# Kernel optimization log

Hardware: AMD Instinct MI355X
Metric: run time of the kernel (lower is better)

Reference implementation:

```python
import jax, jax.numpy as jnp
import numpy as np

B, S, D, H, AD, E = 4, 2048, 1024, 2048, 128, 8

def _ln(x, g, b, eps=1e-5):
    m = jnp.mean(x, axis=-1, keepdims=True)
    v = jnp.var(x, axis=-1, keepdims=True)
    return (x - m) * jax.lax.rsqrt(v + eps) * g + b

def setup_inputs() -> dict:
    key = jax.random.key(0)
    ks = jax.random.split(key, 12)
    scale = 1.0 / D ** 0.5
    ascale = scale * 0.01
    ead = 0.01 / AD ** 0.5
    return {
        'x': jax.random.normal(ks[0], (B, S, D), jnp.float32),
        'expert_weights': jax.random.uniform(ks[1], (B, S, E), jnp.float32),
        'Wu': jax.random.normal(ks[2], (H, D), jnp.float32) * scale,
        'bu': jnp.zeros((H,), jnp.float32),
        'Wg': jax.random.normal(ks[3], (H, D), jnp.float32) * scale,
        'bg': jnp.zeros((H,), jnp.float32),
        'Wd': jax.random.normal(ks[4], (D, H), jnp.float32) * scale,
        'bd': jnp.zeros((D,), jnp.float32),
        'Wpre': jax.random.normal(ks[5], (AD, D), jnp.float32) * ascale,
        'bpre': jnp.zeros((AD,), jnp.float32),
        'Wpost': jax.random.normal(ks[6], (AD, H), jnp.float32) * ascale,
        'bpost': jnp.zeros((AD,), jnp.float32),
        'ln_g': jnp.ones((AD,), jnp.float32),
        'ln_b': jnp.zeros((AD,), jnp.float32),
        'Wap': jax.random.normal(ks[7], (H, AD), jnp.float32) * ascale,
        'A': jax.random.normal(ks[8], (E, AD, AD), jnp.float32) * ead,
        'eg': jnp.ones((E, AD), jnp.float32),
        'eb': jnp.zeros((E, AD), jnp.float32),
        'Wp': jax.random.normal(ks[9], (H, AD), jnp.float32) * ead,
        'Wo': jax.random.normal(ks[10], (D, H), jnp.float32) * ead,
    }

def reference(x, expert_weights, Wu, bu, Wg, bg, Wd, bd, Wpre, bpre, Wpost, bpost, ln_g, ln_b, Wap, A, eg, eb, Wp, Wo):
    # ---- SharedExpertMLP ----
    up = x @ Wu.T + bu                      # [B,S,H]
    gate = x @ Wg.T + bg
    hidden = jax.nn.silu(gate) * up
    adapt_in = _ln(x @ Wpre.T + bpre, ln_g, ln_b)        # [B,S,AD]
    adapt_out = _ln(hidden @ Wpost.T + bpost, ln_g, ln_b)
    aw = jnp.einsum('bsa,bta->bst', adapt_in, adapt_out)  # [B,S,S]
    aw = jax.nn.silu(jnp.clip(aw, -5.0, 5.0))
    adapt = jnp.einsum('bst,bta->bsa', aw, adapt_in)
    hidden = hidden + 0.1 * (adapt @ Wap.T)
    shared = hidden @ Wd.T + bd                           # [B,S,D]
    # ---- expert branch (vectorized over experts) ----
    pre = x @ Wpre.T + bpre                               # [B,S,AD] (no adapt_norm here, as in torch)
    h = jnp.einsum('bsa,eca->ebsc', pre, A)               # per-expert adapter linear
    h = _ln(h, eg[:, None, None, :], eb[:, None, None, :])
    wmask = jnp.where(expert_weights > 0, expert_weights, 0.0)  # [B,S,E]
    hw = jnp.einsum('ebsa,bse->bsa', h, wmask)            # weighted combine before shared projections
    Wc = Wo @ Wp                                          # [D,AD]: output_proj(expert_proj(.))
    contrib = hw @ Wc.T                                   # [B,S,D]
    # sum_i w_i * (shared + 0.1*mask_i*expert_i) = shared*sum(w) + 0.1*sum(w_i*expert_i)
    return shared * jnp.sum(expert_weights, axis=-1, keepdims=True) + 0.1 * contrib
```

## Files before the change

kernel.cpp:

```cpp
#include <hip/hip_runtime.h>
#include <math.h>

#define BB 4
#define SS 2048
#define DD 1024
#define HH 2048
#define AD 128
#define EE 8
#define MM (BB*SS)
#define PS 136

typedef unsigned short u16;
typedef short bf16x8 __attribute__((ext_vector_type(8)));
typedef float f32x4 __attribute__((ext_vector_type(4)));
typedef float f32x16 __attribute__((ext_vector_type(16)));

__device__ __forceinline__ float silu_f(float x){ return x / (1.f + __expf(-x)); }

__device__ __forceinline__ u16 f2bf(float f){
    union { float f; unsigned u; } c; c.f = f;
    unsigned r = (c.u + 0x7FFFu + ((c.u >> 16) & 1u)) >> 16;
    return (u16)r;
}

__device__ __forceinline__ void gld16(const u16* g, u16* l){
    __builtin_amdgcn_global_load_lds((const __attribute__((address_space(1))) void*)g,
                                     (__attribute__((address_space(3))) void*)l, 16, 0, 0);
}

#define VMCNT(n) asm volatile("s_waitcnt vmcnt(" #n ")" ::: "memory")

__global__ __launch_bounds__(256,2) void mfma_sk(
    const u16* __restrict__ A, const u16* __restrict__ B, float* __restrict__ P,
    int M, int K, int S, long sA, long sB, long sC, long sSplit)
{
    __shared__ __align__(16) u16 As[128*32];
    __shared__ __align__(16) u16 Bs[128*32];
    const int t = threadIdx.x;
    const int lane = t & 63;
    const int wv = t >> 6;
    const int s = blockIdx.x;
    const int m0 = blockIdx.y * 128;
    const u16* Ab = A + (long)blockIdx.z * sA;
    const u16* Bb = B + (long)blockIdx.z * sB;
    const int srow = t >> 2, scol = (t & 3) * 8;
    const int Ks = K / S, kBeg = s * Ks;
    const u16* ga0 = Ab + (long)(m0 + srow) * K + scol + kBeg;
    const u16* ga1 = ga0 + 64L * K;
    const u16* gb0 = Bb + (long)srow * K + scol + kBeg;
    const u16* gb1 = gb0 + 64L * K;
    u16* la0 = As + t * 8;  u16* la1 = As + 2048 + t * 8;
    u16* lb0 = Bs + t * 8;  u16* lb1 = Bs + 2048 + t * 8;
    const int fr = lane & 15, q = lane >> 4;
    const int wm = (wv & 1) * 64, wn = (wv >> 1) * 64;

    f32x4 acc[4][4] = {};
    for (int k0 = 0; k0 < Ks; k0 += 32) {
        gld16(ga0 + k0, la0);
        gld16(ga1 + k0, la1);
        gld16(gb0 + k0, lb0);
        gld16(gb1 + k0, lb1);
        __syncthreads();
        bf16x8 af[4], bfr[4];
        #pragma unroll
        for (int i = 0; i < 4; ++i) af[i]  = *(const bf16x8*)&As[(wm + i*16 + fr)*32 + q*8];
        #pragma unroll
        for (int i = 0; i < 4; ++i) bfr[i] = *(const bf16x8*)&Bs[(wn + i*16 + fr)*32 + q*8];
        #pragma unroll
        for (int mi = 0; mi < 4; ++mi)
            #pragma unroll
            for (int ni = 0; ni < 4; ++ni)
                acc[mi][ni] = __builtin_amdgcn_mfma_f32_16x16x32_bf16(af[mi], bfr[ni], acc[mi][ni], 0, 0, 0);
        __syncthreads();
    }

    float* Pf = P + (long)s * sSplit + (long)blockIdx.z * sC;
    #pragma unroll
    for (int mi = 0; mi < 4; ++mi)
        #pragma unroll
        for (int ni = 0; ni < 4; ++ni) {
            const int col = wn + ni*16 + fr;
            #pragma unroll
            for (int r = 0; r < 4; ++r) {
                const int row = m0 + wm + mi*16 + q*4 + r;
                Pf[(long)row * 128 + col] = acc[mi][ni][r];
            }
        }
}

__global__ __launch_bounds__(512,2) void mfma_upgate(
    const u16* __restrict__ X, const u16* __restrict__ Wu_, const u16* __restrict__ Wg_,
    const float* __restrict__ bu, const float* __restrict__ bg, u16* __restrict__ H)
{
    __shared__ __align__(16) u16 lds[65536];
    const int t = threadIdx.x, lane = t & 63, wv = t >> 6;
    const int l31 = lane & 31, kh = lane >> 5;
    const int wr = wv >> 2, wc = wv & 3;
    const int m0 = blockIdx.y * 256, n0 = blockIdx.x * 128;

    const int srow = t >> 2;
    const int gcol = (((t & 3) ^ ((t >> 3) & 3)) * 8);
    const u16* gx0 = X   + (long)(m0 + srow) * DD + gcol;
    const u16* gx1 = gx0 + 128L * DD;
    const u16* gu  = Wu_ + (long)(n0 + srow) * DD + gcol;
    const u16* gg  = Wg_ + (long)(n0 + srow) * DD + gcol;
    const int st8 = t * 8;

    const int sw3 = (l31 >> 1) & 3;
    int offA[4][2], offB[2];
    #pragma unroll
    for (int m = 0; m < 4; ++m)
        #pragma unroll
        for (int ks = 0; ks < 2; ++ks)
            offA[m][ks] = (wr*128 + m*32 + l31)*32 + (((ks*2 + kh) ^ sw3) * 8);
    #pragma unroll
    for (int ks = 0; ks < 2; ++ks)
        offB[ks] = (wc*32 + l31)*32 + (((ks*2 + kh) ^ sw3) * 8);

    f32x16 accU[4] = {};
    f32x16 accG[4] = {};

    auto stage = [&](int tb) {
        u16* Lb = lds + (tb & 3) * 16384;
        const int k0 = tb * 32;
        gld16(gx0 + k0, Lb + st8);
        gld16(gx1 + k0, Lb + 4096 + st8);
        gld16(gu  + k0, Lb + 8192 + st8);
        gld16(gg  + k0, Lb + 12288 + st8);
    };

    auto compute = [&](int tb) {
        const u16* Lb = lds + (tb & 3) * 16384;
        bf16x8 a[4][2], uf[2], gf[2];
        #pragma unroll
        for (int ks = 0; ks < 2; ++ks) {
            uf[ks] = *(const bf16x8*)&Lb[8192  + offB[ks]];
            gf[ks] = *(const bf16x8*)&Lb[12288 + offB[ks]];
        }
        #pragma unroll
        for (int m = 0; m < 4; ++m)
            #pragma unroll
            for (int ks = 0; ks < 2; ++ks)
                a[m][ks] = *(const bf16x8*)&Lb[offA[m][ks]];
        __builtin_amdgcn_s_setprio(1);
        #pragma unroll
        for (int m = 0; m < 4; ++m)
            #pragma unroll
            for (int ks = 0; ks < 2; ++ks) {
                accU[m] = __builtin_amdgcn_mfma_f32_32x32x16_bf16(a[m][ks], uf[ks], accU[m], 0, 0, 0);
                accG[m] = __builtin_amdgcn_mfma_f32_32x32x16_bf16(a[m][ks], gf[ks], accG[m], 0, 0, 0);
            }
        __builtin_amdgcn_s_setprio(0);
    };

    stage(0); stage(1); stage(2);

    #pragma unroll 1
    for (int tt = 0; tt < 29; ++tt) {
        VMCNT(8);
        __builtin_amdgcn_s_barrier();
        __builtin_amdgcn_sched_barrier(0);
        stage(tt + 3);
        compute(tt);
    }
    VMCNT(8);
    __builtin_amdgcn_s_barrier();
    __builtin_amdgcn_sched_barrier(0);
    compute(29);
    VMCNT(4);
    __builtin_amdgcn_s_barrier();
    __builtin_amdgcn_sched_barrier(0);
    compute(30);
    VMCNT(0);
    __builtin_amdgcn_s_barrier();
    __builtin_amdgcn_sched_barrier(0);
    compute(31);

    const int col = n0 + wc*32 + l31;
    const float bub = bu[col], bgb = bg[col];
    u16* Hp = H + (long)(m0 + wr*128) * HH + col;
    #pragma unroll
    for (int m = 0; m < 4; ++m)
        #pragma unroll
        for (int r = 0; r < 16; ++r) {
            const int rowl = m*32 + (r & 3) + 8*(r >> 2) + 4*kh;
            const float u = accU[m][r] + bub;
            const float g = accG[m][r] + bgb;
            Hp[(long)rowl * HH] = f2bf(silu_f(g) * u);
        }
}

__global__ __launch_bounds__(256,2) void mfma_final(
    const u16* __restrict__ Hh, const u16* __restrict__ Wd_,
    const u16* __restrict__ Ac, const u16* __restrict__ Wcat,
    const float* __restrict__ bd, const float* __restrict__ sumw,
    float* __restrict__ out)
{
    __shared__ __align__(16) u16 As[128*32];
    __shared__ __align__(16) u16 Bs[128*32];
    const int t = threadIdx.x, lane = t & 63, wv = t >> 6;
    const int m0 = blockIdx.y * 128, n0 = blockIdx.x * 128;
    const int srow = t >> 2, scol = (t & 3) * 8;
    const int l31 = lane & 31, kh = lane >> 5;
    const int wm = (wv & 1) * 64, wn = (wv >> 1) * 64;
    u16* la0 = As + t * 8;  u16* la1 = As + 2048 + t * 8;
    u16* lb0 = Bs + t * 8;  u16* lb1 = Bs + 2048 + t * 8;

    f32x16 acc[2][2] = {};
    {
        const u16* ga0 = Hh  + (long)(m0 + srow) * HH + scol;
        const u16* ga1 = ga0 + 64L * HH;
        const u16* gb0 = Wd_ + (long)(n0 + srow) * HH + scol;
        const u16* gb1 = gb0 + 64L * HH;
        for (int k0 = 0; k0 < HH; k0 += 32) {
            gld16(ga0 + k0, la0);
            gld16(ga1 + k0, la1);
            gld16(gb0 + k0, lb0);
            gld16(gb1 + k0, lb1);
            __syncthreads();
            bf16x8 af[2][2], bf[2][2];
            #pragma unroll
            for (int mt = 0; mt < 2; ++mt)
                #pragma unroll
                for (int ks = 0; ks < 2; ++ks) {
                    af[mt][ks] = *(const bf16x8*)&As[(wm + mt*32 + l31)*32 + ks*16 + kh*8];
                    bf[mt][ks] = *(const bf16x8*)&Bs[(wn + mt*32 + l31)*32 + ks*16 + kh*8];
                }
            #pragma unroll
            for (int mt = 0; mt < 2; ++mt)
                #pragma unroll
                for (int nt = 0; nt < 2; ++nt)
                    #pragma unroll
                    for (int ks = 0; ks < 2; ++ks)
                        acc[mt][nt] = __builtin_amdgcn_mfma_f32_32x32x16_bf16(af[mt][ks], bf[nt][ks], acc[mt][nt], 0, 0, 0);
            __syncthreads();
        }
    }
    f32x16 acc2[2][2] = {};
    {
        const u16* ga0 = Ac   + (long)(m0 + srow) * 256 + scol;
        const u16* ga1 = ga0 + 64L * 256;
        const u16* gb0 = Wcat + (long)(n0 + srow) * 256 + scol;
        const u16* gb1 = gb0 + 64L * 256;
        for (int k0 = 0; k0 < 256; k0 += 32) {
            gld16(ga0 + k0, la0);
            gld16(ga1 + k0, la1);
            gld16(gb0 + k0, lb0);
            gld16(gb1 + k0, lb1);
            __syncthreads();
            bf16x8 af[2][2], bf[2][2];
            #pragma unroll
            for (int mt = 0; mt < 2; ++mt)
                #pragma unroll
                for (int ks = 0; ks < 2; ++ks) {
                    af[mt][ks] = *(const bf16x8*)&As[(wm + mt*32 + l31)*32 + ks*16 + kh*8];
                    bf[mt][ks] = *(const bf16x8*)&Bs[(wn + mt*32 + l31)*32 + ks*16 + kh*8];
                }
            #pragma unroll
            for (int mt = 0; mt < 2; ++mt)
                #pragma unroll
                for (int nt = 0; nt < 2; ++nt)
                    #pragma unroll
                    for (int ks = 0; ks < 2; ++ks)
                        acc2[mt][nt] = __builtin_amdgcn_mfma_f32_32x32x16_bf16(af[mt][ks], bf[nt][ks], acc2[mt][nt], 0, 0, 0);
            __syncthreads();
        }
    }
    #pragma unroll
    for (int mt = 0; mt < 2; ++mt)
        #pragma unroll
        for (int nt = 0; nt < 2; ++nt) {
            const int col = n0 + wn + nt*32 + l31;
            #pragma unroll
            for (int r = 0; r < 16; ++r) {
                const int row = m0 + wm + mt*32 + (r & 3) + 8*(r >> 2) + 4*kh;
                out[(long)row * DD + col] =
                    sumw[row] * (acc[mt][nt][r] + bd[col]) + 0.1f * acc2[mt][nt][r];
            }
        }
}

__global__ __launch_bounds__(256,2) void flash_pv(
    const u16* __restrict__ ai, const u16* __restrict__ ao,
    const u16* __restrict__ aiT, float* __restrict__ adaptP)
{
    __shared__ __align__(16) u16 As[128*32];
    __shared__ __align__(16) u16 Bs[128*32];
    __shared__ __align__(16) u16 Psh[128*PS];
    const int t = threadIdx.x, lane = t & 63, wv = t >> 6;
    const int fr = lane & 15, q = lane >> 4;
    const int wm = (wv & 1) * 64, wn = (wv >> 1) * 64;
    const int tg = blockIdx.x, s0 = blockIdx.y * 128, b = blockIdx.z;
    const u16* aib  = ai  + (long)b * SS * AD;
    const u16* aob  = ao  + (long)b * SS * AD;
    const u16* aiTb = aiT + (long)b * AD * SS;
    const int srow = t >> 2, scol = (t & 3) * 8;
    u16* la0 = As + t * 8;  u16* la1 = As + 2048 + t * 8;
    u16* lb0 = Bs + t * 8;  u16* lb1 = Bs + 2048 + t * 8;
    const u16* ga0 = aib + (long)(s0 + srow) * AD + scol;
    const u16* ga1 = ga0 + 64L * AD;

    f32x4 vacc[4][4] = {};
    for (int ti = 0; ti < 2; ++ti) {
        const int t0 = tg * 256 + ti * 128;
        const u16* gb0 = aob + (long)(t0 + srow) * AD + scol;
        const u16* gb1 = gb0 + 64L * AD;
        f32x4 acc[4][4] = {};
        for (int k0 = 0; k0 < AD; k0 += 32) {
            gld16(ga0 + k0, la0);
            gld16(ga1 + k0, la1);
            gld16(gb0 + k0, lb0);
            gld16(gb1 + k0, lb1);
            __syncthreads();
            bf16x8 af[4], bfr[4];
            #pragma unroll
            for (int i = 0; i < 4; ++i) af[i]  = *(const bf16x8*)&As[(wm + i*16 + fr)*32 + q*8];
            #pragma unroll
            for (int i = 0; i < 4; ++i) bfr[i] = *(const bf16x8*)&Bs[(wn + i*16 + fr)*32 + q*8];
            #pragma unroll
            for (int mi = 0; mi < 4; ++mi)
                #pragma unroll
                for (int ni = 0; ni < 4; ++ni)
                    acc[mi][ni] = __builtin_amdgcn_mfma_f32_16x16x32_bf16(af[mi], bfr[ni], acc[mi][ni], 0, 0, 0);
            __syncthreads();
        }
        #pragma unroll
        for (int mi = 0; mi < 4; ++mi)
            #pragma unroll
            for (int ni = 0; ni < 4; ++ni)
                #pragma unroll
                for (int r = 0; r < 4; ++r) {
                    float v = acc[mi][ni][r];
                    v = fminf(fmaxf(v, -5.f), 5.f);
                    Psh[(wm + mi*16 + q*4 + r)*PS + wn + ni*16 + fr] = f2bf(silu_f(v));
                }
        __syncthreads();
        #pragma unroll
        for (int kk = 0; kk < 4; ++kk) {
            bf16x8 pf[4], bi[4];
            #pragma unroll
            for (int mi = 0; mi < 4; ++mi)
                pf[mi] = *(const bf16x8*)&Psh[(wm + mi*16 + fr)*PS + kk*32 + q*8];
            #pragma unroll
            for (int ni = 0; ni < 4; ++ni)
                bi[ni] = *(const bf16x8*)&aiTb[(long)(wn + ni*16 + fr)*SS + t0 + kk*32 + q*8];
            #pragma unroll
            for (int mi = 0; mi < 4; ++mi)
                #pragma unroll
                for (int ni = 0; ni < 4; ++ni)
                    vacc[mi][ni] = __builtin_amdgcn_mfma_f32_16x16x32_bf16(pf[mi], bi[ni], vacc[mi][ni], 0, 0, 0);
        }
    }
    float* Pf = adaptP + (long)tg * MM * AD + (long)(b * SS + s0) * AD;
    #pragma unroll
    for (int mi = 0; mi < 4; ++mi)
        #pragma unroll
        for (int ni = 0; ni < 4; ++ni) {
            const int col = wn + ni*16 + fr;
            #pragma unroll
            for (int r = 0; r < 4; ++r) {
                const int row = wm + mi*16 + q*4 + r;
                Pf[(long)row * AD + col] = vacc[mi][ni][r];
            }
        }
}

__global__ __launch_bounds__(256) void scale_adapt(
    const float* __restrict__ P, const float* __restrict__ sumw, u16* __restrict__ acat)
{
    const int i = blockIdx.x * 256 + threadIdx.x;
    float4 v = ((const float4*)P)[i];
    #pragma unroll
    for (int tg = 1; tg < 8; ++tg) {
        const float4 w = ((const float4*)P)[i + (long)tg * (MM*AD/4)];
        v.x += w.x; v.y += w.y; v.z += w.z; v.w += w.w;
    }
    const long grow = i >> 5;
    const float sw = sumw[grow];
    ushort4 o;
    o.x = f2bf(sw*v.x); o.y = f2bf(sw*v.y); o.z = f2bf(sw*v.z); o.w = f2bf(sw*v.w);
    ((ushort4*)acat)[grow*64 + 32 + (i & 31)] = o;
}

__global__ __launch_bounds__(256) void expert_fused(
    const u16* __restrict__ pre, const u16* __restrict__ aexp,
    const float* __restrict__ ew, const float* __restrict__ eg,
    const float* __restrict__ eb, u16* __restrict__ acat,
    float* __restrict__ sumw)
{
    __shared__ float ewsh[64*8];
    __shared__ float egsh[8*128], ebsh[8*128];
    const int t = threadIdx.x, lane = t & 63, wv = t >> 6;
    const int fr = lane & 15, q = lane >> 4;
    const int wm = wv * 16;
    const int m0 = blockIdx.x * 64;
    if (t < 128) {
        const int row = t >> 1, j = (t & 1)*4;
        *(float4*)&ewsh[row*8+j] = *(const float4*)&ew[(long)(m0+row)*EE + j];
    }
    {   const int e = t >> 5, c = (t & 31)*4;
        *(float4*)&egsh[e*128+c] = *(const float4*)&eg[e*128+c];
        *(float4*)&ebsh[e*128+c] = *(const float4*)&eb[e*128+c]; }
    __syncthreads();

    f32x4 hwacc[8] = {};
    for (int e = 0; e < EE; ++e) {
        f32x4 acc[8] = {};
        const u16* Ae = aexp + (long)e * AD * AD;
        #pragma unroll
        for (int ks = 0; ks < 4; ++ks) {
            bf16x8 af, bfr[8];
            af = *(const bf16x8*)&pre[(long)(m0 + wm + fr)*AD + ks*32 + q*8];
            #pragma unroll
            for (int ni = 0; ni < 8; ++ni)
                bfr[ni] = *(const bf16x8*)&Ae[(long)(ni*16 + fr)*AD + ks*32 + q*8];
            #pragma unroll
            for (int ni = 0; ni < 8; ++ni)
                acc[ni] = __builtin_amdgcn_mfma_f32_16x16x32_bf16(af, bfr[ni], acc[ni], 0, 0, 0);
        }
        #pragma unroll
        for (int r = 0; r < 4; ++r) {
            float s = 0.f, s2 = 0.f;
            #pragma unroll
            for (int ni = 0; ni < 8; ++ni) { const float v = acc[ni][r]; s += v; s2 += v*v; }
            #pragma unroll
            for (int msk = 1; msk < 16; msk <<= 1) {
                s  += __shfl_xor(s,  msk, 64);
                s2 += __shfl_xor(s2, msk, 64);
            }
            const float mean = s * (1.f/128.f);
            const float var  = s2 * (1.f/128.f) - mean*mean;
            const float rs   = rsqrtf(var + 1e-5f);
            const int rowl = wm + q*4 + r;
            float w = ewsh[rowl*8 + e]; w = w > 0.f ? w : 0.f;
            #pragma unroll
            for (int ni = 0; ni < 8; ++ni) {
                const int col = ni*16 + fr;
                hwacc[ni][r] += w * ((acc[ni][r] - mean) * rs * egsh[e*128+col] + ebsh[e*128+col]);
            }
        }
    }
    #pragma unroll
    for (int r = 0; r < 4; ++r) {
        const int rowl = wm + q*4 + r;
        #pragma unroll
        for (int ni = 0; ni < 8; ++ni)
            acat[(long)(m0+rowl)*256 + ni*16 + fr] = f2bf(hwacc[ni][r]);
        if (fr == 0) {
            float sw = 0.f;
            #pragma unroll
            for (int j = 0; j < 8; ++j) sw += ewsh[rowl*8 + j];
            sumw[m0 + rowl] = sw;
        }
    }
}

template<int S>
__global__ __launch_bounds__(128) void ln_reduce(
    const float* __restrict__ P, long sSplit, const float* __restrict__ bias,
    u16* __restrict__ raw, u16* __restrict__ ln_out,
    const float* __restrict__ g, const float* __restrict__ b)
{
    const int r = blockIdx.x, tid = threadIdx.x;
    float v = bias[tid];
    #pragma unroll
    for (int s = 0; s < S; ++s) v += P[(long)s * sSplit + (long)r * AD + tid];
    if (raw) raw[(long)r * AD + tid] = f2bf(v);
    __shared__ float red[AD], red2[AD];
    red[tid] = v; red2[tid] = v*v;
    __syncthreads();
    for (int s = 64; s > 0; s >>= 1) {
        if (tid < s) { red[tid] += red[tid+s]; red2[tid] += red2[tid+s]; }
        __syncthreads();
    }
    const float mean = red[0] * (1.f/AD);
    const float var  = red2[0] * (1.f/AD) - mean*mean;
    const float rs   = rsqrtf(var + 1e-5f);
    ln_out[(long)r * AD + tid] = f2bf((v - mean) * rs * g[tid] + b[tid]);
}

__global__ __launch_bounds__(256) void reduce_cat(
    const float* __restrict__ P, u16* __restrict__ Wcat)
{
    const int i = blockIdx.x * 256 + threadIdx.x;
    const int a4 = i & 31, z = (i >> 5) & 1, d = i >> 6;
    const float* src = P + (long)z * (4L*DD*AD) + (long)d * AD + a4*4;
    float4 v = *(const float4*)src;
    #pragma unroll
    for (int s = 1; s < 4; ++s) {
        const float4 w = *(const float4*)(src + (long)s * DD * AD);
        v.x += w.x; v.y += w.y; v.z += w.z; v.w += w.w;
    }
    ushort4 o; o.x=f2bf(v.x); o.y=f2bf(v.y); o.z=f2bf(v.z); o.w=f2bf(v.w);
    ((ushort4*)Wcat)[(long)d*64 + z*32 + a4] = o;
}

__global__ __launch_bounds__(256) void transpose6(
    const u16* __restrict__ wRaw, u16* __restrict__ wT,
    const u16* __restrict__ ai, u16* __restrict__ aiT)
{
    __shared__ u16 tile[32][33];
    const int z = blockIdx.z;
    const u16* in; u16* out;
    if (z < 2) { in = wRaw + (long)z * HH * AD; out = wT + (long)z * AD * HH; }
    else       { in = ai + (long)(z-2) * SS * AD; out = aiT + (long)(z-2) * AD * SS; }
    const int x0 = blockIdx.x * 32, y0 = blockIdx.y * 32;
    const int tx = threadIdx.x & 31, ty = threadIdx.x >> 5;
    #pragma unroll
    for (int j = 0; j < 4; ++j)
        tile[ty + j*8][tx] = in[(long)(y0 + ty + j*8) * AD + x0 + tx];
    __syncthreads();
    #pragma unroll
    for (int j = 0; j < 4; ++j)
        out[(long)(x0 + ty + j*8) * SS + y0 + tx] = tile[tx][ty + j*8];
}

struct Cvt5 { const float* in[5]; u16* out[5]; long cum[6]; };
__global__ __launch_bounds__(256) void cvt_pack(Cvt5 a)
{
    const long i = (long)blockIdx.x * 256 + threadIdx.x;
    if (i >= a.cum[5]) return;
    int s = 0;
    while (i >= a.cum[s+1]) ++s;
    const long j = i - a.cum[s];
    const float4 v = ((const float4*)a.in[s])[j];
    ushort4 o;
    o.x = f2bf(v.x); o.y = f2bf(v.y); o.z = f2bf(v.z); o.w = f2bf(v.w);
    ((ushort4*)a.out[s])[j] = o;
}

extern "C" void kernel_launch(void* const* d_in, const int* in_sizes, int n_in,
                              void* d_out, int out_size, void* d_ws, size_t ws_size,
                              hipStream_t stream) {
    const float* x    = (const float*)d_in[0];
    const float* ew   = (const float*)d_in[1];
    const float* Wu   = (const float*)d_in[2];
    const float* bu   = (const float*)d_in[3];
    const float* Wg   = (const float*)d_in[4];
    const float* bg   = (const float*)d_in[5];
    const float* Wd   = (const float*)d_in[6];
    const float* bd   = (const float*)d_in[7];
    const float* Wpre = (const float*)d_in[8];
    const float* bpre = (const float*)d_in[9];
    const float* Wpost= (const float*)d_in[10];
    const float* bpost= (const float*)d_in[11];
    const float* ln_g = (const float*)d_in[12];
    const float* ln_b = (const float*)d_in[13];
    const float* Wap  = (const float*)d_in[14];
    const float* Aex  = (const float*)d_in[15];
    const float* eg   = (const float*)d_in[16];
    const float* eb   = (const float*)d_in[17];
    const float* Wp   = (const float*)d_in[18];
    const float* Wo   = (const float*)d_in[19];
    float* out = (float*)d_out;

    char* p = (char*)d_ws;
    auto take = [&](long bytes) -> char* {
        char* r = p; p += (bytes + 255) & ~255L; return r;
    };
    u16* x_slot  = (u16*)take(16777216);
    u16* wslot   = (u16*)take((long)2*DD*HH*2);
    u16* wpre    = (u16*)take((long)AD*DD*2);
    u16* aex     = (u16*)take((long)EE*AD*AD*2);
    u16* pre_bf  = (u16*)take((long)MM*AD*2);
    u16* ai_bf   = (u16*)take((long)MM*AD*2);
    char* shareA = take(33554432);
    u16* acat    = (u16*)take((long)MM*256*2);
    float* sumw  = (float*)take((long)MM*4);
    u16* hidden  = (u16*)take((long)MM*HH*2);

    u16* x_bf    = x_slot;
    u16* aiT     = x_slot;
    u16* wRaw    = aiT  + 1048576;
    u16* wT      = wRaw + 524288;
    u16* wpost_w = wT   + 524288;
    u16* wcat    = wpost_w + 262144;
    u16* ao_bf   = wcat + 262144;
    float* wcP   = (float*)(ao_bf + 1048576);
    float* preP   = (float*)shareA;
    float* wpostP = (float*)shareA;
    float* adaptP = (float*)shareA;

    {
        Cvt5 a;
        a.in[0]=x;    a.out[0]=x_bf;              long n0=(long)MM*DD/4;
        a.in[1]=Wu;   a.out[1]=wslot;             long n1=(long)HH*DD/4;
        a.in[2]=Wg;   a.out[2]=wslot+(long)DD*HH; long n2=(long)HH*DD/4;
        a.in[3]=Wpre; a.out[3]=wpre;              long n3=(long)AD*DD/4;
        a.in[4]=Aex;  a.out[4]=aex;               long n4=(long)EE*AD*AD/4;
        a.cum[0]=0; a.cum[1]=n0; a.cum[2]=n0+n1; a.cum[3]=n0+n1+n2;
        a.cum[4]=n0+n1+n2+n3; a.cum[5]=n0+n1+n2+n3+n4;
        cvt_pack<<<dim3((a.cum[5]+255)/256), 256, 0, stream>>>(a);
    }
    mfma_sk<<<dim3(4, MM/128, 1), 256, 0, stream>>>(
        x_bf, wpre, preP, MM, DD, 4, 0, 0, 0, (long)MM*AD);
    ln_reduce<4><<<dim3(MM), 128, 0, stream>>>(preP, (long)MM*AD, bpre, pre_bf, ai_bf, ln_g, ln_b);
    expert_fused<<<dim3(MM/64), 256, 0, stream>>>(pre_bf, aex, ew, eg, eb, acat, sumw);
    mfma_upgate<<<dim3(HH/128, MM/256), 512, 0, stream>>>(
        x_bf, wslot, wslot+(long)DD*HH, bu, bg, hidden);
    {
        Cvt5 a;
        a.in[0]=Wo;    a.out[0]=wslot;             long n0=(long)DD*HH/4;
        a.in[1]=Wd;    a.out[1]=wslot+(long)DD*HH; long n1=(long)DD*HH/4;
        a.in[2]=Wpost; a.out[2]=wpost_w;           long n2=(long)AD*HH/4;
        a.in[3]=Wp;    a.out[3]=wRaw;              long n3=(long)HH*AD/4;
        a.in[4]=Wap;   a.out[4]=wRaw+(long)HH*AD;  long n4=(long)HH*AD/4;
        a.cum[0]=0; a.cum[1]=n0; a.cum[2]=n0+n1; a.cum[3]=n0+n1+n2;
        a.cum[4]=n0+n1+n2+n3; a.cum[5]=n0+n1+n2+n3+n4;
        cvt_pack<<<dim3((a.cum[5]+255)/256), 256, 0, stream>>>(a);
    }
    transpose6<<<dim3(4,64,6), 256, 0, stream>>>(wRaw, wT, ai_bf, aiT);
    mfma_sk<<<dim3(4, DD/128, 2), 256, 0, stream>>>(
        wslot, wT, wcP, DD, HH, 4, (long)DD*HH, (long)AD*HH, 4L*DD*AD, (long)DD*AD);
    reduce_cat<<<dim3(256), 256, 0, stream>>>(wcP, wcat);
    mfma_sk<<<dim3(8, MM/128, 1), 256, 0, stream>>>(
        hidden, wpost_w, wpostP, MM, HH, 8, 0, 0, 0, (long)MM*AD);
    ln_reduce<8><<<dim3(MM), 128, 0, stream>>>(wpostP, (long)MM*AD, bpost, nullptr, ao_bf, ln_g, ln_b);
    flash_pv<<<dim3(8, SS/128, BB), 256, 0, stream>>>(ai_bf, ao_bf, aiT, adaptP);
    scale_adapt<<<dim3((long)MM*AD/4/256), 256, 0, stream>>>(adaptP, sumw, acat);
    mfma_final<<<dim3(DD/128, MM/128), 256, 0, stream>>>(
        hidden, wslot+(long)DD*HH, acat, wcat, bd, sumw, out);
}
```

Baseline: 430.8 us.

## Interleave Wu/Wg rows and retile up-gate GEMM to 256x256 with 16x16 MFMA

Measured after the change: 443.0 us. 1.03x slower.

```diff
diff --git a/kernel.cpp b/kernel.cpp
--- a/kernel.cpp
+++ b/kernel.cpp
@@ -89,104 +89,134 @@
 }
 
 __global__ __launch_bounds__(512,2) void mfma_upgate(
-    const u16* __restrict__ X, const u16* __restrict__ Wu_, const u16* __restrict__ Wg_,
+    const u16* __restrict__ X, const u16* __restrict__ W,
     const float* __restrict__ bu, const float* __restrict__ bg, u16* __restrict__ H)
 {
     __shared__ __align__(16) u16 lds[65536];
     const int t = threadIdx.x, lane = t & 63, wv = t >> 6;
-    const int l31 = lane & 31, kh = lane >> 5;
+    const int fr = lane & 15, q = lane >> 4;
     const int wr = wv >> 2, wc = wv & 3;
-    const int m0 = blockIdx.y * 256, n0 = blockIdx.x * 128;
-
-    const int srow = t >> 2;
-    const int gcol = (((t & 3) ^ ((t >> 3) & 3)) * 8);
-    const u16* gx0 = X   + (long)(m0 + srow) * DD + gcol;
-    const u16* gx1 = gx0 + 128L * DD;
-    const u16* gu  = Wu_ + (long)(n0 + srow) * DD + gcol;
-    const u16* gg  = Wg_ + (long)(n0 + srow) * DD + gcol;
+
+    const int flat = blockIdx.y * 16 + blockIdx.x;
+    const int swz = (flat & 7) * 64 + (flat >> 3);
+    const int m0 = (swz >> 4) * 256, n0 = (swz & 15) * 256;
+
+    const int r0 = t >> 3, c8 = t & 7;
+    const int csw = c8 ^ ((r0 >> 1) & 7);
+    const u16* gA = X + (long)(m0 + r0) * DD + csw * 8;
+    const u16* gB = W + (long)(n0 + r0) * DD + csw * 8;
     const int st8 = t * 8;
 
-    const int sw3 = (l31 >> 1) & 3;
-    int offA[4][2], offB[2];
-    #pragma unroll
-    for (int m = 0; m < 4; ++m)
+    const int sA = (fr >> 1) & 7;
+    int koff[2];
+    koff[0] = (q ^ sA) * 8;
+    koff[1] = ((4 + q) ^ sA) * 8;
+    const int aB = wr * 8192;
+    const int bB = 16384 + (wc >> 1) * 8192;
+    const int cb = (wc & 1) * 64;
+
+    f32x4 acc[8][4] = {};
+    bf16x8 af[8][2], bf[2][2];
+
+    auto stageA = [&](int tk, int h) {
+        u16* Lb = lds + (tk & 1) * 32768 + h * 8192;
+        const u16* g = gA + (long)(h * 128) * DD + tk * 64;
+        gld16(g, Lb + st8);
+        gld16(g + 64L * DD, Lb + 4096 + st8);
+    };
+    auto stageB = [&](int tk, int h) {
+        u16* Lb = lds + (tk & 1) * 32768 + 16384 + h * 8192;
+        const u16* g = gB + (long)(h * 128) * DD + tk * 64;
+        gld16(g, Lb + st8);
+        gld16(g + 64L * DD, Lb + 4096 + st8);
+    };
+    auto readA = [&](const u16* Lb, int mq0) {
+        #pragma unroll
+        for (int mm = 0; mm < 4; ++mm)
+            #pragma unroll
+            for (int ks = 0; ks < 2; ++ks)
+                af[mq0+mm][ks] = *(const bf16x8*)&Lb[aB + ((mq0+mm)*16 + fr)*64 + koff[ks]];
+    };
+    auto readB = [&](const u16* Lb, int nb) {
+        #pragma unroll
+        for (int nn = 0; nn < 2; ++nn)
+            #pragma unroll
+            for (int ks = 0; ks < 2; ++ks)
+                bf[nn][ks] = *(const bf16x8*)&Lb[bB + (cb + (nb+nn)*16 + fr)*64 + koff[ks]];
+    };
+    auto quad = [&](int mq0, int nq0) {
+        __builtin_amdgcn_s_setprio(1);
         #pragma unroll
         for (int ks = 0; ks < 2; ++ks)
-            offA[m][ks] = (wr*128 + m*32 + l31)*32 + (((ks*2 + kh) ^ sw3) * 8);
-    #pragma unroll
-    for (int ks = 0; ks < 2; ++ks)
-        offB[ks] = (wc*32 + l31)*32 + (((ks*2 + kh) ^ sw3) * 8);
-
-    f32x16 accU[4] = {};
-    f32x16 accG[4] = {};
-
-    auto stage = [&](int tb) {
-        u16* Lb = lds + (tb & 3) * 16384;
-        const int k0 = tb * 32;
-        gld16(gx0 + k0, Lb + st8);
-        gld16(gx1 + k0, Lb + 4096 + st8);
-        gld16(gu  + k0, Lb + 8192 + st8);
-        gld16(gg  + k0, Lb + 12288 + st8);
-    };
-
-    auto compute = [&](int tb) {
-        const u16* Lb = lds + (tb & 3) * 16384;
-        bf16x8 a[4][2], uf[2], gf[2];
-        #pragma unroll
-        for (int ks = 0; ks < 2; ++ks) {
-            uf[ks] = *(const bf16x8*)&Lb[8192  + offB[ks]];
-            gf[ks] = *(const bf16x8*)&Lb[12288 + offB[ks]];
-        }
-        #pragma unroll
-        for (int m = 0; m < 4; ++m)
-            #pragma unroll
-            for (int ks = 0; ks < 2; ++ks)
-                a[m][ks] = *(const bf16x8*)&Lb[offA[m][ks]];
-        __builtin_amdgcn_s_setprio(1);
-        #pragma unroll
-        for (int m = 0; m < 4; ++m)
-            #pragma unroll
-            for (int ks = 0; ks < 2; ++ks) {
-                accU[m] = __builtin_amdgcn_mfma_f32_32x32x16_bf16(a[m][ks], uf[ks], accU[m], 0, 0, 0);
-                accG[m] = __builtin_amdgcn_mfma_f32_32x32x16_bf16(a[m][ks], gf[ks], accG[m], 0, 0, 0);
-            }
+            #pragma unroll
+            for (int mm = 0; mm < 4; ++mm)
+                #pragma unroll
+                for (int nn = 0; nn < 2; ++nn)
+                    acc[mq0+mm][nq0+nn] = __builtin_amdgcn_mfma_f32_16x16x32_bf16(
+                        af[mq0+mm][ks], bf[nn][ks], acc[mq0+mm][nq0+nn], 0, 0, 0);
         __builtin_amdgcn_s_setprio(0);
     };
 
-    stage(0); stage(1); stage(2);
-
-    #pragma unroll 1
-    for (int tt = 0; tt < 29; ++tt) {
-        VMCNT(8);
-        __builtin_amdgcn_s_barrier();
-        __builtin_amdgcn_sched_barrier(0);
-        stage(tt + 3);
-        compute(tt);
-    }
-    VMCNT(8);
-    __builtin_amdgcn_s_barrier();
-    __builtin_amdgcn_sched_barrier(0);
-    compute(29);
+    stageA(0,0); stageA(0,1); stageB(0,0); stageB(0,1); stageA(1,0); stageA(1,1);
     VMCNT(4);
     __builtin_amdgcn_s_barrier();
     __builtin_amdgcn_sched_barrier(0);
-    compute(30);
-    VMCNT(0);
-    __builtin_amdgcn_s_barrier();
-    __builtin_amdgcn_sched_barrier(0);
-    compute(31);
-
-    const int col = n0 + wc*32 + l31;
-    const float bub = bu[col], bgb = bg[col];
-    u16* Hp = H + (long)(m0 + wr*128) * HH + col;
-    #pragma unroll
-    for (int m = 0; m < 4; ++m)
-        #pragma unroll
-        for (int r = 0; r < 16; ++r) {
-            const int rowl = m*32 + (r & 3) + 8*(r >> 2) + 4*kh;
-            const float u = accU[m][r] + bub;
-            const float g = accG[m][r] + bgb;
-            Hp[(long)rowl * HH] = f2bf(silu_f(g) * u);
+
+    #pragma unroll 1
+    for (int kt = 0; kt < 16; ++kt) {
+        const u16* Lb = lds + (kt & 1) * 32768;
+        readA(Lb, 0); readB(Lb, 0);
+        if (kt < 15) stageB(kt+1, 0);
+        __builtin_amdgcn_sched_barrier(0);
+        __builtin_amdgcn_s_barrier();
+        quad(0, 0);
+        __builtin_amdgcn_s_barrier();
+        __builtin_amdgcn_sched_barrier(0);
+        readA(Lb, 4);
+        if (kt < 15) stageB(kt+1, 1);
+        __builtin_amdgcn_sched_barrier(0);
+        __builtin_amdgcn_s_barrier();
+        quad(4, 0);
+        __builtin_amdgcn_s_barrier();
+        __builtin_amdgcn_sched_barrier(0);
+        readB(Lb, 2);
+        if (kt < 14) stageA(kt+2, 0);
+        __builtin_amdgcn_sched_barrier(0);
+        __builtin_amdgcn_s_barrier();
+        quad(0, 2);
+        __builtin_amdgcn_s_barrier();
+        __builtin_amdgcn_sched_barrier(0);
+        if (kt < 14) stageA(kt+2, 1);
+        if (kt == 14) { VMCNT(0); } else { VMCNT(4); }
+        __builtin_amdgcn_sched_barrier(0);
+        __builtin_amdgcn_s_barrier();
+        quad(4, 2);
+        __builtin_amdgcn_s_barrier();
+        __builtin_amdgcn_sched_barrier(0);
+    }
+
+    const int colI = n0 + wc*64 + fr;
+    float myb[4];
+    #pragma unroll
+    for (int n = 0; n < 4; ++n) {
+        const int ch = (colI + n*16) >> 1;
+        myb[n] = (lane & 1) ? bg[ch] : bu[ch];
+    }
+    u16* Hp = H + (long)(m0 + wr*128) * HH;
+    #pragma unroll
+    for (int mq = 0; mq < 8; ++mq)
+        #pragma unroll
+        for (int n = 0; n < 4; ++n) {
+            const int ch = (colI + n*16) >> 1;
+            #pragma unroll
+            for (int r = 0; r < 4; ++r) {
+                float v = acc[mq][n][r] + myb[n];
+                const float o = __shfl_xor(v, 1, 64);
+                if (!(lane & 1)) {
+                    const int row = mq*16 + q*4 + r;
+                    Hp[(long)row * HH + ch] = f2bf(silu_f(o) * v);
+                }
+            }
         }
 }
 
@@ -527,6 +557,20 @@
     ushort4 o;
     o.x = f2bf(v.x); o.y = f2bf(v.y); o.z = f2bf(v.z); o.w = f2bf(v.w);
     ((ushort4*)a.out[s])[j] = o;
+}
+
+__global__ __launch_bounds__(256) void cvt_wuwg(
+    const float* __restrict__ Wu, const float* __restrict__ Wg, u16* __restrict__ out)
+{
+    const long i = (long)blockIdx.x * 256 + threadIdx.x;
+    const int row = (int)(i >> 8), c4 = (int)(i & 255);
+    const float4 u = ((const float4*)Wu)[i];
+    const float4 g = ((const float4*)Wg)[i];
+    ushort4 ou, og;
+    ou.x=f2bf(u.x); ou.y=f2bf(u.y); ou.z=f2bf(u.z); ou.w=f2bf(u.w);
+    og.x=f2bf(g.x); og.y=f2bf(g.y); og.z=f2bf(g.z); og.w=f2bf(g.w);
+    ((ushort4*)out)[(long)(2*row)*256 + c4]   = ou;
+    ((ushort4*)out)[(long)(2*row+1)*256 + c4] = og;
 }
 
 extern "C" void kernel_launch(void* const* d_in, const int* in_sizes, int n_in,
@@ -584,20 +628,20 @@
     {
         Cvt5 a;
         a.in[0]=x;    a.out[0]=x_bf;              long n0=(long)MM*DD/4;
-        a.in[1]=Wu;   a.out[1]=wslot;             long n1=(long)HH*DD/4;
-        a.in[2]=Wg;   a.out[2]=wslot+(long)DD*HH; long n2=(long)HH*DD/4;
-        a.in[3]=Wpre; a.out[3]=wpre;              long n3=(long)AD*DD/4;
-        a.in[4]=Aex;  a.out[4]=aex;               long n4=(long)EE*AD*AD/4;
+        a.in[1]=Wpre; a.out[1]=wpre;              long n1=(long)AD*DD/4;
+        a.in[2]=Aex;  a.out[2]=aex;               long n2=(long)EE*AD*AD/4;
+        a.in[3]=x;    a.out[3]=x_bf;
+        a.in[4]=x;    a.out[4]=x_bf;
         a.cum[0]=0; a.cum[1]=n0; a.cum[2]=n0+n1; a.cum[3]=n0+n1+n2;
-        a.cum[4]=n0+n1+n2+n3; a.cum[5]=n0+n1+n2+n3+n4;
+        a.cum[4]=n0+n1+n2; a.cum[5]=n0+n1+n2;
         cvt_pack<<<dim3((a.cum[5]+255)/256), 256, 0, stream>>>(a);
+        cvt_wuwg<<<dim3((long)HH*DD/4/256), 256, 0, stream>>>(Wu, Wg, wslot);
     }
     mfma_sk<<<dim3(4, MM/128, 1), 256, 0, stream>>>(
         x_bf, wpre, preP, MM, DD, 4, 0, 0, 0, (long)MM*AD);
     ln_reduce<4><<<dim3(MM), 128, 0, stream>>>(preP, (long)MM*AD, bpre, pre_bf, ai_bf, ln_g, ln_b);
     expert_fused<<<dim3(MM/64), 256, 0, stream>>>(pre_bf, aex, ew, eg, eb, acat, sumw);
-    mfma_upgate<<<dim3(HH/128, MM/256), 512, 0, stream>>>(
-        x_bf, wslot, wslot+(long)DD*HH, bu, bg, hidden);
+    mfma_upgate<<<dim3(16, 32), 512, 0, stream>>>(x_bf, wslot, bu, bg, hidden);
     {
         Cvt5 a;
         a.in[0]=Wo;    a.out[0]=wslot;             long n0=(long)DD*HH/4;
```

## Rewrite final GEMM with 256x128 tiles, 4-stage async pipeline and swizzled LDS

Applied to the files above, without the earlier changes.

Result: no change. 424.2 us (-1.5%).

```diff
diff --git a/kernel.cpp b/kernel.cpp
--- a/kernel.cpp
+++ b/kernel.cpp
@@ -190,93 +190,105 @@
         }
 }
 
-__global__ __launch_bounds__(256,2) void mfma_final(
+__global__ __launch_bounds__(512,2) void mfma_final(
     const u16* __restrict__ Hh, const u16* __restrict__ Wd_,
     const u16* __restrict__ Ac, const u16* __restrict__ Wcat,
     const float* __restrict__ bd, const float* __restrict__ sumw,
     float* __restrict__ out)
 {
-    __shared__ __align__(16) u16 As[128*32];
-    __shared__ __align__(16) u16 Bs[128*32];
+    __shared__ __align__(16) u16 lds[49152];
     const int t = threadIdx.x, lane = t & 63, wv = t >> 6;
-    const int m0 = blockIdx.y * 128, n0 = blockIdx.x * 128;
-    const int srow = t >> 2, scol = (t & 3) * 8;
     const int l31 = lane & 31, kh = lane >> 5;
-    const int wm = (wv & 1) * 64, wn = (wv >> 1) * 64;
-    u16* la0 = As + t * 8;  u16* la1 = As + 2048 + t * 8;
-    u16* lb0 = Bs + t * 8;  u16* lb1 = Bs + 2048 + t * 8;
-
-    f32x16 acc[2][2] = {};
-    {
-        const u16* ga0 = Hh  + (long)(m0 + srow) * HH + scol;
-        const u16* ga1 = ga0 + 64L * HH;
-        const u16* gb0 = Wd_ + (long)(n0 + srow) * HH + scol;
-        const u16* gb1 = gb0 + 64L * HH;
-        for (int k0 = 0; k0 < HH; k0 += 32) {
-            gld16(ga0 + k0, la0);
-            gld16(ga1 + k0, la1);
-            gld16(gb0 + k0, lb0);
-            gld16(gb1 + k0, lb1);
-            __syncthreads();
-            bf16x8 af[2][2], bf[2][2];
-            #pragma unroll
-            for (int mt = 0; mt < 2; ++mt)
-                #pragma unroll
-                for (int ks = 0; ks < 2; ++ks) {
-                    af[mt][ks] = *(const bf16x8*)&As[(wm + mt*32 + l31)*32 + ks*16 + kh*8];
-                    bf[mt][ks] = *(const bf16x8*)&Bs[(wn + mt*32 + l31)*32 + ks*16 + kh*8];
-                }
-            #pragma unroll
-            for (int mt = 0; mt < 2; ++mt)
-                #pragma unroll
-                for (int nt = 0; nt < 2; ++nt)
-                    #pragma unroll
-                    for (int ks = 0; ks < 2; ++ks)
-                        acc[mt][nt] = __builtin_amdgcn_mfma_f32_32x32x16_bf16(af[mt][ks], bf[nt][ks], acc[mt][nt], 0, 0, 0);
-            __syncthreads();
-        }
-    }
-    f32x16 acc2[2][2] = {};
-    {
-        const u16* ga0 = Ac   + (long)(m0 + srow) * 256 + scol;
-        const u16* ga1 = ga0 + 64L * 256;
-        const u16* gb0 = Wcat + (long)(n0 + srow) * 256 + scol;
-        const u16* gb1 = gb0 + 64L * 256;
-        for (int k0 = 0; k0 < 256; k0 += 32) {
-            gld16(ga0 + k0, la0);
-            gld16(ga1 + k0, la1);
-            gld16(gb0 + k0, lb0);
-            gld16(gb1 + k0, lb1);
-            __syncthreads();
-            bf16x8 af[2][2], bf[2][2];
-            #pragma unroll
-            for (int mt = 0; mt < 2; ++mt)
-                #pragma unroll
-                for (int ks = 0; ks < 2; ++ks) {
-                    af[mt][ks] = *(const bf16x8*)&As[(wm + mt*32 + l31)*32 + ks*16 + kh*8];
-                    bf[mt][ks] = *(const bf16x8*)&Bs[(wn + mt*32 + l31)*32 + ks*16 + kh*8];
-                }
-            #pragma unroll
-            for (int mt = 0; mt < 2; ++mt)
-                #pragma unroll
-                for (int nt = 0; nt < 2; ++nt)
-                    #pragma unroll
-                    for (int ks = 0; ks < 2; ++ks)
-                        acc2[mt][nt] = __builtin_amdgcn_mfma_f32_32x32x16_bf16(af[mt][ks], bf[nt][ks], acc2[mt][nt], 0, 0, 0);
-            __syncthreads();
-        }
-    }
-    #pragma unroll
-    for (int mt = 0; mt < 2; ++mt)
-        #pragma unroll
-        for (int nt = 0; nt < 2; ++nt) {
-            const int col = n0 + wn + nt*32 + l31;
-            #pragma unroll
-            for (int r = 0; r < 16; ++r) {
-                const int row = m0 + wm + mt*32 + (r & 3) + 8*(r >> 2) + 4*kh;
-                out[(long)row * DD + col] =
-                    sumw[row] * (acc[mt][nt][r] + bd[col]) + 0.1f * acc2[mt][nt][r];
-            }
+    const int wr = wv >> 2, wc = wv & 3;
+    const int m0 = blockIdx.y * 256, n0 = blockIdx.x * 128;
+
+    const int r0 = t >> 2;
+    const int gcol = (((t & 3) ^ ((t >> 3) & 3)) * 8);
+    const u16* gA1 = Hh   + (long)(m0 + r0) * HH  + gcol;
+    const u16* gB1 = Wd_  + (long)(n0 + r0) * HH  + gcol;
+    const u16* gA2 = Ac   + (long)(m0 + r0) * 256 + gcol;
+    const u16* gB2 = Wcat + (long)(n0 + r0) * 256 + gcol;
+    const int st8 = t * 8;
+
+    const int sw3 = (l31 >> 1) & 3;
+    int offA[4][2], offB[2];
+    #pragma unroll
+    for (int m = 0; m < 4; ++m)
+        #pragma unroll
+        for (int ks = 0; ks < 2; ++ks)
+            offA[m][ks] = (wr*128 + m*32 + l31)*32 + (((ks*2 + kh) ^ sw3) * 8);
+    #pragma unroll
+    for (int ks = 0; ks < 2; ++ks)
+        offB[ks] = 8192 + (wc*32 + l31)*32 + (((ks*2 + kh) ^ sw3) * 8);
+
+    f32x16 acc[4]  = {};
+    f32x16 acc2[4] = {};
+
+    auto stage = [&](int tk) {
+        u16* Lb = lds + (tk & 3) * 12288;
+        if (tk < 64) {
+            const int k0 = tk * 32;
+            gld16(gA1 + k0,             Lb + st8);
+            gld16(gA1 + 128L*HH + k0,   Lb + 4096 + st8);
+            gld16(gB1 + k0,             Lb + 8192 + st8);
+        } else {
+            const int k0 = (tk - 64) * 32;
+            gld16(gA2 + k0,             Lb + st8);
+            gld16(gA2 + 128L*256 + k0,  Lb + 4096 + st8);
+            gld16(gB2 + k0,             Lb + 8192 + st8);
+        }
+    };
+
+    auto compute = [&](int tk, f32x16 (&A)[4]) {
+        const u16* Lb = lds + (tk & 3) * 12288;
+        bf16x8 a[4][2], b[2];
+        #pragma unroll
+        for (int ks = 0; ks < 2; ++ks) b[ks] = *(const bf16x8*)&Lb[offB[ks]];
+        #pragma unroll
+        for (int m = 0; m < 4; ++m)
+            #pragma unroll
+            for (int ks = 0; ks < 2; ++ks)
+                a[m][ks] = *(const bf16x8*)&Lb[offA[m][ks]];
+        __builtin_amdgcn_s_setprio(1);
+        #pragma unroll
+        for (int m = 0; m < 4; ++m)
+            #pragma unroll
+            for (int ks = 0; ks < 2; ++ks)
+                A[m] = __builtin_amdgcn_mfma_f32_32x32x16_bf16(a[m][ks], b[ks], A[m], 0, 0, 0);
+        __builtin_amdgcn_s_setprio(0);
+    };
+
+    stage(0); stage(1); stage(2);
+    #pragma unroll 1
+    for (int tt = 0; tt < 69; ++tt) {
+        VMCNT(6);
+        __builtin_amdgcn_s_barrier();
+        __builtin_amdgcn_sched_barrier(0);
+        stage(tt + 3);
+        if (tt < 64) compute(tt, acc); else compute(tt, acc2);
+    }
+    VMCNT(6);
+    __builtin_amdgcn_s_barrier();
+    __builtin_amdgcn_sched_barrier(0);
+    compute(69, acc2);
+    VMCNT(3);
+    __builtin_amdgcn_s_barrier();
+    __builtin_amdgcn_sched_barrier(0);
+    compute(70, acc2);
+    VMCNT(0);
+    __builtin_amdgcn_s_barrier();
+    __builtin_amdgcn_sched_barrier(0);
+    compute(71, acc2);
+
+    const int col = n0 + wc*32 + l31;
+    const float bdc = bd[col];
+    #pragma unroll
+    for (int m = 0; m < 4; ++m)
+        #pragma unroll
+        for (int r = 0; r < 16; ++r) {
+            const int row = m0 + wr*128 + m*32 + (r & 3) + 8*(r >> 2) + 4*kh;
+            out[(long)row * DD + col] =
+                sumw[row] * (acc[m][r] + bdc) + 0.1f * acc2[m][r];
         }
 }
 
@@ -618,6 +630,6 @@
     ln_reduce<8><<<dim3(MM), 128, 0, stream>>>(wpostP, (long)MM*AD, bpost, nullptr, ao_bf, ln_g, ln_b);
     flash_pv<<<dim3(8, SS/128, BB), 256, 0, stream>>>(ai_bf, ao_bf, aiT, adaptP);
     scale_adapt<<<dim3((long)MM*AD/4/256), 256, 0, stream>>>(adaptP, sumw, acat);
-    mfma_final<<<dim3(DD/128, MM/128), 256, 0, stream>>>(
+    mfma_final<<<dim3(DD/128, MM/256), 512, 0, stream>>>(
         hidden, wslot+(long)DD*HH, acat, wcat, bd, sumw, out);
 }
```
